# Performance work log

Measured on AMD Instinct MI355X. Metric: run time of the kernel, lower is better.

The kernel has to match this reference:

```python
import jax, jax.numpy as jnp
import numpy as np

TEMPERATURE = 0.1
BASE_TEMPERATURE = 0.07
EPS = 1e-10


def setup_inputs() -> dict:
    key = jax.random.key(0)
    k1, k2 = jax.random.split(key)
    # feats_: [total_classes=64, n_view=128, feat_dim=256] sampled anchor features
    feats_ = jax.random.normal(k1, (64, 128, 256), dtype=jnp.float32)
    # labels_: class id per anchor group (21-class dataset -> repeats across groups)
    labels_ = jax.random.randint(k2, (64,), 0, 21, dtype=jnp.int32)
    return {"feats_": feats_, "labels_": labels_}


def reference(feats_, labels_):
    anchor_num, n_view, d = feats_.shape
    N = anchor_num * n_view
    # torch.cat(torch.unbind(feats_, dim=1), dim=0): view-major flattening
    cf = jnp.transpose(feats_, (1, 0, 2)).reshape(N, d)  # [N, d]
    # labels for the flattened ordering (mask.repeat tiles the [A,A] eq-mask)
    big_labels = jnp.tile(labels_, n_view)  # [N]

    logits = jnp.matmul(cf, cf.T) / TEMPERATURE  # [N, N]
    logits = logits - jax.lax.stop_gradient(jnp.max(logits, axis=1, keepdims=True))

    mask = (big_labels[:, None] == big_labels[None, :]).astype(jnp.float32)
    neg_mask = 1.0 - mask                       # negatives BEFORE removing diagonal
    mask = mask * (1.0 - jnp.eye(N, dtype=jnp.float32))  # positives exclude self

    exp_logits = jnp.exp(logits)
    neg_logits = jnp.sum(exp_logits * neg_mask, axis=1, keepdims=True)  # [N, 1]
    log_prob = logits - jnp.log(exp_logits + neg_logits + EPS)
    mean_log_prob_pos = jnp.sum(mask * log_prob, axis=1) / jnp.sum(mask, axis=1)
    loss = jnp.mean(-(TEMPERATURE / BASE_TEMPERATURE) * mean_log_prob_pos)
    return loss
```

## Files before the change

### kernel.cpp

```cpp
#include <hip/hip_runtime.h>
#include <hip/hip_bf16.h>

#define N_ROWS 8192
#define DIM 256
#define NANCH 64
#define NVIEW 128
#define APS 16
#define NPART 8

typedef __attribute__((ext_vector_type(8))) short bf16x8;
typedef __attribute__((ext_vector_type(4))) float f32x4;
typedef __attribute__((ext_vector_type(16))) float f32x16;
typedef __attribute__((ext_vector_type(4))) float float4v;
typedef __attribute__((ext_vector_type(4))) unsigned short ushort4v;

__device__ __forceinline__ unsigned short f2bf(float x) {
  union { float f; unsigned int u; } c; c.f = x;
  unsigned int u = c.u;
  unsigned int r = (u + 0x7fffu + ((u >> 16) & 1u)) >> 16;
  return (unsigned short)r;
}

__device__ __forceinline__ float bf2f(unsigned short b) {
  union { unsigned int u; float f; } c; c.u = ((unsigned int)b) << 16;
  return c.f;
}

__device__ __forceinline__ void gload_lds16(const void* g, void* l) {
  __builtin_amdgcn_global_load_lds(
      (const __attribute__((address_space(1))) unsigned int*)g,
      (__attribute__((address_space(3))) unsigned int*)l, 16, 0, 0);
}

__global__ void cast_diag_kernel(const float4v* __restrict__ in,
                                 ushort4v* __restrict__ out,
                                 float* __restrict__ diag) {
  const int w = threadIdx.x >> 6;
  const int l = threadIdx.x & 63;
  const int row = blockIdx.x * 4 + w;
  const float s = 3.16227766016838f;
  float4v v = in[row * 64 + l];
  ushort4v o;
  o.x = f2bf(v.x * s);
  o.y = f2bf(v.y * s);
  o.z = f2bf(v.z * s);
  o.w = f2bf(v.w * s);
  out[row * 64 + l] = o;
  float c0 = bf2f(o.x), c1 = bf2f(o.y), c2 = bf2f(o.z), c3 = bf2f(o.w);
  float ss = c0 * c0 + c1 * c1 + c2 * c2 + c3 * c3;
#pragma unroll
  for (int st = 1; st < 64; st <<= 1) ss += __shfl_xor(ss, st);
  if (l == 0) diag[row] = ss;
}

__global__ __launch_bounds__(512, 4) void pcl_negsum(
    const unsigned short* __restrict__ Xb, const int* __restrict__ labels,
    const float* __restrict__ diag, float* __restrict__ ns_partial) {
  const int rb = blockIdx.x & 63;
  const int part = blockIdx.x >> 6;
  const int strip = part >> 1;
  const int half = part & 1;
  const int tid = threadIdx.x;
  const int wid = tid >> 6;
  const int lane = tid & 63;
  const int l31 = lane & 31;
  const int khalf = lane >> 5;
  const int rg = wid >> 1;
  const int cg = wid & 1;

  __shared__ unsigned short buf[2][64 * DIM];
  __shared__ float sns[8][32];
  __shared__ float sdiag[128];
  __shared__ int slab[NANCH];

  if (tid < NANCH) slab[tid] = labels[tid];
  if (tid >= 128 && tid < 256) sdiag[tid - 128] = diag[rb * 128 + tid - 128];
  __syncthreads();
  const int myLab = slab[rb];

  bf16x8 afrag[16];
#pragma unroll
  for (int ks = 0; ks < 16; ++ks) {
    const unsigned short* p =
        Xb + (size_t)(rb * 128 + rg * 32 + l31) * DIM + ks * 16 + khalf * 8;
    afrag[ks] = *(const bf16x8*)p;
    asm volatile("" : "+v"(afrag[ks]));
  }

  float thr;
  {
    float d = sdiag[rg * 32 + l31];
#pragma unroll
    for (int st = 1; st < 32; st <<= 1) d = fminf(d, __shfl_xor(d, st));
    thr = d - 40.f;
  }

  float ns[16];
#pragma unroll
  for (int r = 0; r < 16; ++r) ns[r] = 0.f;

  int srcoff[4];
#pragma unroll
  for (int i = 0; i < 4; ++i) srcoff[i] = lane * DIM + (i * 8 + wid) * 8;
  const int ldsbase = wid * 1024;

  const int boff = khalf * 1024 + cg * 512 + l31 * 16;

  const unsigned short* asrc0 =
      Xb + ((size_t)(strip * APS) * NVIEW + half * 64) * DIM;

#pragma unroll
  for (int i = 0; i < 4; ++i)
    gload_lds16(asrc0 + srcoff[i], (char*)&buf[0][0] + ldsbase + i * 8192);
  __syncthreads();

  int cb = 0;
  for (int a = 0; a < APS; ++a) {
    if (a + 1 < APS) {
      const unsigned short* src = asrc0 + (size_t)(a + 1) * NVIEW * DIM;
#pragma unroll
      for (int i = 0; i < 4; ++i)
        gload_lds16(src + srcoff[i], (char*)&buf[cb ^ 1][0] + ldsbase + i * 8192);
    }

    const char* bufc = (const char*)&buf[cb][0];
    f32x16 acc = {};
#pragma unroll
    for (int ks = 0; ks < 16; ++ks) {
      bf16x8 bfr = *(const bf16x8*)(bufc + ks * 2048 + boff);
      acc = __builtin_amdgcn_mfma_f32_32x32x16_bf16(afrag[ks], bfr, acc, 0, 0, 0);
    }

    if (slab[strip * APS + a] != myLab) {
      float vmax = acc[0];
#pragma unroll
      for (int r = 1; r < 16; ++r) vmax = fmaxf(vmax, acc[r]);
      if (__builtin_expect(__any(vmax > thr), 0)) {
#pragma unroll
        for (int r = 0; r < 16; ++r) {
          const int rr = (r & 3) + 8 * (r >> 2) + 4 * khalf;
          float mr = sdiag[rg * 32 + rr];
          float v = acc[r];
          if (v > mr - 40.f) ns[r] += __expf(v - mr);
        }
      }
    }
    __syncthreads();
    cb ^= 1;
  }

#pragma unroll
  for (int r = 0; r < 16; ++r) {
#pragma unroll
    for (int st = 1; st < 32; st <<= 1) ns[r] += __shfl_xor(ns[r], st);
  }
  if (l31 == 0) {
#pragma unroll
    for (int r = 0; r < 16; ++r) {
      const int rr = (r & 3) + 8 * (r >> 2) + 4 * khalf;
      sns[wid][rr] = ns[r];
    }
  }
  __syncthreads();
  if (tid < 128) {
    const int rg2 = tid >> 5, rr = tid & 31;
    ns_partial[part * N_ROWS + rb * 128 + tid] =
        sns[rg2 * 2 + 0][rr] + sns[rg2 * 2 + 1][rr];
  }
}

__global__ __launch_bounds__(512, 4) void pcl_pos(
    const unsigned short* __restrict__ Xb, const int* __restrict__ labels,
    const float* __restrict__ diag, const float* __restrict__ ns_partial,
    float* __restrict__ partials) {
  const int blk = blockIdx.x;
  const int r0 = blk * 32;
  const int tid = threadIdx.x;
  const int wid = tid >> 6;
  const int lane = tid & 63;
  const int lo = lane & 15;
  const int hi = lane >> 4;
  const int cq = wid & 3;
  const int bq = wid >> 2;

  __shared__ int slab[NANCH];
  __shared__ float sred[8][32];
  __shared__ float smf[32];
  __shared__ float snsf[32];
  __shared__ int poslist[NANCH];
  __shared__ int scnt;

  if (tid < NANCH) slab[tid] = labels[tid];
  if (tid >= 64 && tid < 96) {
    int r = tid - 64;
    smf[r] = diag[r0 + r];
    float s = 0.f;
#pragma unroll
    for (int p = 0; p < NPART; ++p) s += ns_partial[p * N_ROWS + r0 + r];
    snsf[r] = s;
  }
  if (tid == 0) {
    int La0 = labels[blk >> 2];
    int c = 0;
    for (int b = 0; b < NANCH; ++b)
      if (labels[b] == La0) poslist[c++] = b;
    scnt = c;
  }
  __syncthreads();

  bf16x8 afrag[2][8];
#pragma unroll
  for (int ri = 0; ri < 2; ++ri) {
#pragma unroll
    for (int ks = 0; ks < 8; ++ks) {
      const unsigned short* p = Xb + (r0 + ri * 16 + lo) * DIM + ks * 32 + hi * 8;
      afrag[ri][ks] = *(const bf16x8*)p;
      asm volatile("" : "+v"(afrag[ri][ks]));
    }
  }

  const int cnt = scnt;
  float pos[8];
#pragma unroll
  for (int t = 0; t < 8; ++t) pos[t] = 0.f;

  for (int p = bq; p < cnt; p += 2) {
    const int b = poslist[p];
    const int c0 = b * NVIEW + cq * 32;
    f32x4 acc[2][2];
#pragma unroll
    for (int ri = 0; ri < 2; ++ri)
#pragma unroll
      for (int ci = 0; ci < 2; ++ci)
        acc[ri][ci] = (f32x4){0.f, 0.f, 0.f, 0.f};

#pragma unroll
    for (int ks = 0; ks < 8; ++ks) {
      bf16x8 b0 = *(const bf16x8*)(Xb + (c0 + lo) * DIM + ks * 32 + hi * 8);
      bf16x8 b1 = *(const bf16x8*)(Xb + (c0 + 16 + lo) * DIM + ks * 32 + hi * 8);
      acc[0][0] = __builtin_amdgcn_mfma_f32_16x16x32_bf16(afrag[0][ks], b0, acc[0][0], 0, 0, 0);
      acc[0][1] = __builtin_amdgcn_mfma_f32_16x16x32_bf16(afrag[0][ks], b1, acc[0][1], 0, 0, 0);
      acc[1][0] = __builtin_amdgcn_mfma_f32_16x16x32_bf16(afrag[1][ks], b0, acc[1][0], 0, 0, 0);
      acc[1][1] = __builtin_amdgcn_mfma_f32_16x16x32_bf16(afrag[1][ks], b1, acc[1][1], 0, 0, 0);
    }

#pragma unroll
    for (int ri = 0; ri < 2; ++ri) {
#pragma unroll
      for (int ci = 0; ci < 2; ++ci) {
#pragma unroll
        for (int reg = 0; reg < 4; ++reg) {
          const int t = ri * 4 + reg;
          const int row = ri * 16 + hi * 4 + reg;
          int grow = r0 + row;
          int gcol = c0 + ci * 16 + lo;
          if (grow != gcol) {
            float d = acc[ri][ci][reg] - smf[row];
            pos[t] += d - __logf(__expf(d) + snsf[row] + 1e-10f);
          }
        }
      }
    }
  }

#pragma unroll
  for (int t = 0; t < 8; ++t) {
#pragma unroll
    for (int st = 1; st < 16; st <<= 1) pos[t] += __shfl_xor(pos[t], st);
  }
  if (lo == 0) {
#pragma unroll
    for (int ri = 0; ri < 2; ++ri)
#pragma unroll
      for (int reg = 0; reg < 4; ++reg)
        sred[wid][ri * 16 + hi * 4 + reg] = pos[ri * 4 + reg];
  }
  __syncthreads();

  const float poscnt = (float)(cnt * NVIEW - 1);
  if (tid < 32) {
    float P = 0.f;
#pragma unroll
    for (int w = 0; w < 8; ++w) P += sred[w][tid];
    smf[tid] = P / poscnt;
  }
  __syncthreads();
  if (tid == 0) {
    float s = 0.f;
    for (int r = 0; r < 32; ++r) s += smf[r];
    partials[blk] = s;
  }
}

__global__ void final_reduce(const float* __restrict__ partials, float* __restrict__ out) {
  __shared__ float s[256];
  int t = threadIdx.x;
  s[t] = partials[t];
  __syncthreads();
  for (int st = 128; st > 0; st >>= 1) {
    if (t < st) s[t] += s[t + st];
    __syncthreads();
  }
  if (t == 0) out[0] = -(0.1f / 0.07f) * s[0] / (float)N_ROWS;
}

extern "C" void kernel_launch(void* const* d_in, const int* in_sizes, int n_in,
                              void* d_out, int out_size, void* d_ws, size_t ws_size,
                              hipStream_t stream) {
  const float* feats = (const float*)d_in[0];
  const int* labels = (const int*)d_in[1];
  float* out = (float*)d_out;

  char* base = (char*)d_ws;
  unsigned short* Xb = (unsigned short*)d_ws;
  float* diag = (float*)(base + (size_t)N_ROWS * DIM * 2);
  float* ns_partial = (float*)(base + (size_t)N_ROWS * DIM * 2 + N_ROWS * 4);
  float* partials = (float*)(base + (size_t)N_ROWS * DIM * 2 + N_ROWS * 4 +
                             NPART * N_ROWS * 4);

  cast_diag_kernel<<<N_ROWS / 4, 256, 0, stream>>>((const float4v*)feats,
                                                   (ushort4v*)Xb, diag);
  pcl_negsum<<<NANCH * NPART, 512, 0, stream>>>(Xb, labels, diag, ns_partial);
  pcl_pos<<<N_ROWS / 32, 512, 0, stream>>>(Xb, labels, diag, ns_partial, partials);
  final_reduce<<<1, 256, 0, stream>>>(partials, out);
}
```

Baseline: 83.52 us.

## Halve negsum block size with 64-row wave tiles and add pos-loss fast path

The negative-sum kernel now runs 256 threads per block. Each wave handles 64 rows using two A-fragment sets, so every LDS B fragment feeds two MFMAs, and the K loop is split over two accumulators to shorten the dependency chains. Per-thread register sums are replaced by shuffle reductions plus LDS atomics on the rare path where the exp threshold is exceeded. The positive-pair kernel precomputes log(negsum) and skips exp/log when the logit difference is very negative, which trades a small approximation for less transcendental work. The extra A fragments and four accumulators raise register pressure, and the lower thread count per block may reduce occupancy.

After: 78.29 us. -6.3%, faster.

```diff
diff --git a/kernel.cpp b/kernel.cpp
--- a/kernel.cpp
+++ b/kernel.cpp
@@ -53,7 +53,7 @@
   if (l == 0) diag[row] = ss;
 }
 
-__global__ __launch_bounds__(512, 4) void pcl_negsum(
+__global__ __launch_bounds__(256, 2) void pcl_negsum(
     const unsigned short* __restrict__ Xb, const int* __restrict__ labels,
     const float* __restrict__ diag, float* __restrict__ ns_partial) {
   const int rb = blockIdx.x & 63;
@@ -68,80 +68,93 @@
   const int rg = wid >> 1;
   const int cg = wid & 1;
 
-  __shared__ unsigned short buf[2][64 * DIM];
-  __shared__ float sns[8][32];
+  __shared__ __align__(16) unsigned short buf[2][64 * DIM];
   __shared__ float sdiag[128];
+  __shared__ float nsacc[128];
   __shared__ int slab[NANCH];
 
   if (tid < NANCH) slab[tid] = labels[tid];
-  if (tid >= 128 && tid < 256) sdiag[tid - 128] = diag[rb * 128 + tid - 128];
+  if (tid < 128) nsacc[tid] = 0.f;
+  if (tid >= 128) sdiag[tid - 128] = diag[rb * 128 + tid - 128];
   __syncthreads();
   const int myLab = slab[rb];
 
-  bf16x8 afrag[16];
-#pragma unroll
-  for (int ks = 0; ks < 16; ++ks) {
-    const unsigned short* p =
-        Xb + (size_t)(rb * 128 + rg * 32 + l31) * DIM + ks * 16 + khalf * 8;
-    afrag[ks] = *(const bf16x8*)p;
-    asm volatile("" : "+v"(afrag[ks]));
+  bf16x8 afrag[2][16];
+#pragma unroll
+  for (int ri = 0; ri < 2; ++ri) {
+#pragma unroll
+    for (int ks = 0; ks < 16; ++ks) {
+      const unsigned short* p =
+          Xb + (size_t)(rb * 128 + rg * 64 + ri * 32 + l31) * DIM + ks * 16 + khalf * 8;
+      afrag[ri][ks] = *(const bf16x8*)p;
+      asm volatile("" : "+v"(afrag[ri][ks]));
+    }
   }
 
   float thr;
   {
-    float d = sdiag[rg * 32 + l31];
-#pragma unroll
-    for (int st = 1; st < 32; st <<= 1) d = fminf(d, __shfl_xor(d, st));
+    float d = sdiag[rg * 64 + lane];
+#pragma unroll
+    for (int st = 1; st < 64; st <<= 1) d = fminf(d, __shfl_xor(d, st));
     thr = d - 40.f;
   }
 
-  float ns[16];
-#pragma unroll
-  for (int r = 0; r < 16; ++r) ns[r] = 0.f;
-
-  int srcoff[4];
-#pragma unroll
-  for (int i = 0; i < 4; ++i) srcoff[i] = lane * DIM + (i * 8 + wid) * 8;
-  const int ldsbase = wid * 1024;
-
-  const int boff = khalf * 1024 + cg * 512 + l31 * 16;
-
+  const int srcbase = lane * DIM + wid * 8;
   const unsigned short* asrc0 =
       Xb + ((size_t)(strip * APS) * NVIEW + half * 64) * DIM;
 
 #pragma unroll
-  for (int i = 0; i < 4; ++i)
-    gload_lds16(asrc0 + srcoff[i], (char*)&buf[0][0] + ldsbase + i * 8192);
-  __syncthreads();
+  for (int i = 0; i < 8; ++i)
+    gload_lds16(asrc0 + srcbase + i * 32, (char*)&buf[0][0] + wid * 1024 + i * 4096);
+  __syncthreads();
+
+  const int boff = khalf * 1024 + cg * 512 + l31 * 16;
 
   int cb = 0;
   for (int a = 0; a < APS; ++a) {
     if (a + 1 < APS) {
       const unsigned short* src = asrc0 + (size_t)(a + 1) * NVIEW * DIM;
 #pragma unroll
-      for (int i = 0; i < 4; ++i)
-        gload_lds16(src + srcoff[i], (char*)&buf[cb ^ 1][0] + ldsbase + i * 8192);
+      for (int i = 0; i < 8; ++i)
+        gload_lds16(src + srcbase + i * 32, (char*)&buf[cb ^ 1][0] + wid * 1024 + i * 4096);
     }
 
     const char* bufc = (const char*)&buf[cb][0];
-    f32x16 acc = {};
+    f32x16 a0A = {}, a0B = {}, a1A = {}, a1B = {};
 #pragma unroll
     for (int ks = 0; ks < 16; ++ks) {
       bf16x8 bfr = *(const bf16x8*)(bufc + ks * 2048 + boff);
-      acc = __builtin_amdgcn_mfma_f32_32x32x16_bf16(afrag[ks], bfr, acc, 0, 0, 0);
+      if (ks < 8) {
+        a0A = __builtin_amdgcn_mfma_f32_32x32x16_bf16(afrag[0][ks], bfr, a0A, 0, 0, 0);
+        a1A = __builtin_amdgcn_mfma_f32_32x32x16_bf16(afrag[1][ks], bfr, a1A, 0, 0, 0);
+      } else {
+        a0B = __builtin_amdgcn_mfma_f32_32x32x16_bf16(afrag[0][ks], bfr, a0B, 0, 0, 0);
+        a1B = __builtin_amdgcn_mfma_f32_32x32x16_bf16(afrag[1][ks], bfr, a1B, 0, 0, 0);
+      }
     }
 
     if (slab[strip * APS + a] != myLab) {
-      float vmax = acc[0];
-#pragma unroll
-      for (int r = 1; r < 16; ++r) vmax = fmaxf(vmax, acc[r]);
+      f32x16 c0 = a0A + a0B;
+      f32x16 c1 = a1A + a1B;
+      float vmax = c0[0];
+#pragma unroll
+      for (int r = 1; r < 16; ++r) vmax = fmaxf(vmax, c0[r]);
+#pragma unroll
+      for (int r = 0; r < 16; ++r) vmax = fmaxf(vmax, c1[r]);
       if (__builtin_expect(__any(vmax > thr), 0)) {
 #pragma unroll
-        for (int r = 0; r < 16; ++r) {
-          const int rr = (r & 3) + 8 * (r >> 2) + 4 * khalf;
-          float mr = sdiag[rg * 32 + rr];
-          float v = acc[r];
-          if (v > mr - 40.f) ns[r] += __expf(v - mr);
+        for (int t2 = 0; t2 < 2; ++t2) {
+#pragma unroll
+          for (int r = 0; r < 16; ++r) {
+            const int rloc = (r & 3) + 8 * (r >> 2) + 4 * khalf;
+            const int row = rg * 64 + t2 * 32 + rloc;
+            float v = t2 ? c1[r] : c0[r];
+            float mr = sdiag[row];
+            float e = (v > mr - 40.f) ? __expf(v - mr) : 0.f;
+#pragma unroll
+            for (int st = 1; st < 32; st <<= 1) e += __shfl_xor(e, st);
+            if (l31 == 0) atomicAdd(&nsacc[row], e);
+          }
         }
       }
     }
@@ -149,24 +162,8 @@
     cb ^= 1;
   }
 
-#pragma unroll
-  for (int r = 0; r < 16; ++r) {
-#pragma unroll
-    for (int st = 1; st < 32; st <<= 1) ns[r] += __shfl_xor(ns[r], st);
-  }
-  if (l31 == 0) {
-#pragma unroll
-    for (int r = 0; r < 16; ++r) {
-      const int rr = (r & 3) + 8 * (r >> 2) + 4 * khalf;
-      sns[wid][rr] = ns[r];
-    }
-  }
-  __syncthreads();
-  if (tid < 128) {
-    const int rg2 = tid >> 5, rr = tid & 31;
-    ns_partial[part * N_ROWS + rb * 128 + tid] =
-        sns[rg2 * 2 + 0][rr] + sns[rg2 * 2 + 1][rr];
-  }
+  if (tid < 128)
+    ns_partial[part * N_ROWS + rb * 128 + tid] = nsacc[tid];
 }
 
 __global__ __launch_bounds__(512, 4) void pcl_pos(
@@ -187,6 +184,7 @@
   __shared__ float sred[8][32];
   __shared__ float smf[32];
   __shared__ float snsf[32];
+  __shared__ float slog[32];
   __shared__ int poslist[NANCH];
   __shared__ int scnt;
 
@@ -198,6 +196,7 @@
 #pragma unroll
     for (int p = 0; p < NPART; ++p) s += ns_partial[p * N_ROWS + r0 + r];
     snsf[r] = s;
+    slog[r] = __logf(s + 1e-10f);
   }
   if (tid == 0) {
     int La0 = labels[blk >> 2];
@@ -256,7 +255,12 @@
           int gcol = c0 + ci * 16 + lo;
           if (grow != gcol) {
             float d = acc[ri][ci][reg] - smf[row];
-            pos[t] += d - __logf(__expf(d) + snsf[row] + 1e-10f);
+            float lp;
+            if (__builtin_expect(d > -45.f, 0))
+              lp = d - __logf(__expf(d) + snsf[row] + 1e-10f);
+            else
+              lp = d - slog[row];
+            pos[t] += lp;
           }
         }
       }
@@ -320,7 +324,7 @@
 
   cast_diag_kernel<<<N_ROWS / 4, 256, 0, stream>>>((const float4v*)feats,
                                                    (ushort4v*)Xb, diag);
-  pcl_negsum<<<NANCH * NPART, 512, 0, stream>>>(Xb, labels, diag, ns_partial);
+  pcl_negsum<<<NANCH * NPART, 256, 0, stream>>>(Xb, labels, diag, ns_partial);
   pcl_pos<<<N_ROWS / 32, 512, 0, stream>>>(Xb, labels, diag, ns_partial, partials);
   final_reduce<<<1, 256, 0, stream>>>(partials, out);
 }
```
